# Kernel optimization log

Hardware: AMD Instinct MI355X
Metric: run time of the kernel (lower is better)

## Reference

```python
import jax, jax.numpy as jnp
import numpy as np
from jax import lax

ROI_H, ROI_W = 3, 3          # args.roi_size
MAP_SCALE = 8.0              # args.map_scale
UPS = 8                      # args.upsample_ratio
RADIUS = 8
C_OUT = 5                    # boxes per image
WH = ROI_H * 2 ** 2 + 1      # 13: correlation weight spatial size


def conv2d(x, w, b=None, pad=0):
    y = lax.conv_general_dilated(x, w, (1, 1), [(pad, pad), (pad, pad)],
                                 dimension_numbers=('NCHW', 'OIHW', 'NCHW'))
    return y if b is None else y + b[None, :, None, None]


def resize_ac(x, oh, ow):
    """Bilinear resize with align_corners=True. x: (N,C,H,W) -> (N,C,oh,ow)."""
    H, W = x.shape[2], x.shape[3]
    def grid(n_in, n_out):
        if n_out == 1:
            c = jnp.zeros((1,), x.dtype)
        else:
            c = jnp.arange(n_out, dtype=x.dtype) * ((n_in - 1) / (n_out - 1))
        i0 = jnp.clip(jnp.floor(c).astype(jnp.int32), 0, n_in - 1)
        i1 = jnp.clip(i0 + 1, 0, n_in - 1)
        return i0, i1, c - i0.astype(x.dtype)
    h0, h1, fh = grid(H, oh)
    w0, w1, fw = grid(W, ow)
    xr = x[:, :, h0, :] * (1 - fh)[None, None, :, None] + x[:, :, h1, :] * fh[None, None, :, None]
    return xr[:, :, :, w0] * (1 - fw)[None, None, None, :] + xr[:, :, :, w1] * fw[None, None, None, :]


def roi_pooling(feat, boxes_np, out_size):
    """feat: (N,C,H,W); boxes_np: host int array (N,M,4) [x_min,y_min,width,height].
    Returns (N,M,C,out_h,out_w). Boxes are integer constants, so the
    per-box Python loop traces to fixed shapes (N*M small)."""
    N, M = feat.shape[0], boxes_np.shape[1]
    out = []
    for i in range(N):
        regs = []
        for j in range(M):
            x_min, y_min, width, height = (int(v) for v in boxes_np[i, j])
            region = feat[i:i + 1, :, y_min:y_min + height + 1, x_min:x_min + width + 1]
            scale = max(height, width) / max(out_size)
            nh = max(int(height / scale), 1)
            nw = max(int(width / scale), 1)
            region = resize_ac(region, nh, nw)
            tp = (out_size[0] - nh) // 2
            lp = (out_size[1] - nw) // 2
            pr = jnp.pad(region, ((0, 0), (0, 0), (tp, out_size[0] - nh - tp),
                                  (lp, out_size[1] - nw - lp)))[0]
            regs.append(pr / (1e-6 + pr.sum()))
        out.append(jnp.stack(regs))
    return jnp.stack(out)


def _fpn_fuse(feats, p):
    f = [feats[0]] + [conv2d(x, p['c1x1_w%d' % k], p['c1x1_b%d' % k])
                      for k, x in enumerate(feats[1:])]
    # up_and_add pairs (uses original f list, not cascaded)
    P = [resize_ac(f[i], f[i - 1].shape[2], f[i - 1].shape[3]) + f[i - 1] for i in (3, 2, 1)]
    # NB: original ModuleList([conv]*3) shares ONE smooth conv across all levels
    P = [conv2d(x, p['smooth_w'], p['smooth_b'], pad=1) for x in P]
    P = list(reversed(P)) + [f[3]]
    H, W = P[0].shape[2], P[0].shape[3]
    P = [P[0]] + [resize_ac(x, H, W) for x in P[1:]]
    x = conv2d(jnp.concatenate(P, axis=1), p['fuse_w'], pad=1)
    # BatchNorm with fresh running stats (mean=0, var=1), eps=1e-5
    x = x / jnp.sqrt(jnp.asarray(1.0 + 1e-5, x.dtype)) * p['bn_g'][None, :, None, None] + p['bn_b'][None, :, None, None]
    return jax.nn.relu(x)


def _forward(x0, x1, x2, x3, c1x1_w0, c1x1_b0, c1x1_w1, c1x1_b1, c1x1_w2, c1x1_b2,
             smooth_w, smooth_b, fuse_w, bn_g, bn_b,
             ll_w1, ll_b1, ll_w2, ll_b2, ll_w3, ll_b3,
             of_w1, of_b1, of_w2, of_b2, of_w3, of_b3, x_example):
    p = dict(c1x1_w0=c1x1_w0, c1x1_b0=c1x1_b0, c1x1_w1=c1x1_w1, c1x1_b1=c1x1_b1,
             c1x1_w2=c1x1_w2, c1x1_b2=c1x1_b2, smooth_w=smooth_w, smooth_b=smooth_b,
             fuse_w=fuse_w, bn_g=bn_g, bn_b=bn_b)
    z1 = _fpn_fuse([x0, x1, x2, x3], p)
    B, C_IN, H, W = z1.shape
    # boxes are integer indices -> host constants (matches boxes.long())
    boxes_np = (np.asarray(jax.device_get(x_example)) / MAP_SCALE).astype(np.int64)

    weights, z_e = [], None
    for i in range(3):
        rs = (ROI_H * 2 ** i + 1, ROI_W * 2 ** i + 1)
        z_e = roi_pooling(z1, boxes_np, rs)                     # (B,5,C_IN,rh,rw)
        aug = jnp.concatenate([z_e, z_e[..., ::-1], z_e[..., ::-1, :],
                               z_e[..., ::-1, ::-1]], axis=1)   # (B,20,C_IN,rh,rw)
        ph = (WH - rs[0]) // 2
        pw = (WH - rs[1]) // 2
        weights.append(jnp.pad(aug, ((0, 0), (0, 0), (0, 0),
                                     (ph, WH - rs[0] - ph), (pw, WH - rs[1] - pw))))
    # weights built under torch.no_grad -> constants
    w_all = lax.stop_gradient(jnp.concatenate(weights, axis=1))  # (B,60,C_IN,13,13)

    conv_map = jnp.zeros((B, C_OUT * 12, H, W), z1.dtype)
    corr = jax.vmap(lambda z, w: conv2d(z[None], w, pad=WH // 2)[0])
    for i in range(3):
        res = corr(z1, w_all[:, i * C_OUT * 4:(i + 1) * C_OUT * 4])  # (B,20,H,W)
        # replicate original (buggy) slice conv_map[b, i:i+20] = ...
        conv_map = conv_map.at[:, i:i + C_OUT * 4].set(res)
    atten = conv_map.mean(axis=1, keepdims=True)

    h = jnp.concatenate([conv_map, z1 * atten], axis=1)          # (B,316,H,W)
    h = jax.nn.relu(conv2d(h, ll_w1, ll_b1, pad=1))
    h = jax.nn.relu(conv2d(h, ll_w2, ll_b2, pad=1))
    out1 = jax.nn.relu(conv2d(h, ll_w3, ll_b3))

    o = jax.nn.relu(conv2d(z1, of_w1, of_b1, pad=1))
    o = jax.nn.relu(conv2d(o, of_w2, of_b2, pad=1))
    o = jax.nn.sigmoid(conv2d(o, of_w3, of_b3))
    offset = (MAP_SCALE * o - MAP_SCALE / 2) * RADIUS

    offset = resize_ac(offset, H * UPS, W * UPS)
    out1 = resize_ac(out1, H * UPS, W * UPS)
    return out1, offset, atten, lax.stop_gradient(z_e)


def setup_inputs() -> dict:
    key = jax.random.key(0)
    ks = jax.random.split(key, 20)
    f32 = jnp.float32
    def w(k, shape):
        return jax.random.normal(k, shape, f32) * 0.01  # torch init std=0.01
    inp = {
        'x0': jax.random.normal(ks[0], (2, 256, 64, 64), f32),
        'x1': jax.random.normal(ks[1], (2, 512, 32, 32), f32),
        'x2': jax.random.normal(ks[2], (2, 1024, 16, 16), f32),
        'x3': jax.random.normal(ks[3], (2, 2048, 8, 8), f32),
    }
    # boxes in pixel coords [x_min, y_min, width, height]; image assumed 512px
    xy = jax.random.randint(ks[4], (2, 5, 2), 0, 280)
    wh = jax.random.randint(ks[5], (2, 5, 2), 16, 144)
    inp['x_example'] = jnp.concatenate([xy, wh], axis=-1).astype(f32)
    inp.update(
        c1x1_w0=w(ks[6], (256, 512, 1, 1)), c1x1_b0=jnp.zeros((256,), f32),
        c1x1_w1=w(ks[7], (256, 1024, 1, 1)), c1x1_b1=jnp.zeros((256,), f32),
        c1x1_w2=w(ks[8], (256, 2048, 1, 1)), c1x1_b2=jnp.zeros((256,), f32),
        smooth_w=w(ks[9], (256, 256, 3, 3)), smooth_b=jnp.zeros((256,), f32),
        fuse_w=w(ks[10], (256, 1024, 3, 3)),
        bn_g=jnp.ones((256,), f32), bn_b=jnp.zeros((256,), f32),
        ll_w1=w(ks[11], (64, 316, 3, 3)), ll_b1=jnp.zeros((64,), f32),
        ll_w2=w(ks[12], (64, 64, 3, 3)), ll_b2=jnp.zeros((64,), f32),
        ll_w3=w(ks[13], (1, 64, 1, 1)), ll_b3=jnp.zeros((1,), f32),
        of_w1=w(ks[14], (64, 256, 3, 3)), of_b1=jnp.zeros((64,), f32),
        of_w2=w(ks[15], (64, 64, 3, 3)), of_b2=jnp.zeros((64,), f32),
        of_w3=w(ks[16], (2, 64, 1, 1)), of_b3=jnp.zeros((2,), f32),
    )
    return inp


def reference(x0, x1, x2, x3, x_example, c1x1_w0, c1x1_b0, c1x1_w1, c1x1_b1,
              c1x1_w2, c1x1_b2, smooth_w, smooth_b, fuse_w, bn_g, bn_b,
              ll_w1, ll_b1, ll_w2, ll_b2, ll_w3, ll_b3,
              of_w1, of_b1, of_w2, of_b2, of_w3, of_b3):
    return _forward(x0, x1, x2, x3, c1x1_w0, c1x1_b0, c1x1_w1, c1x1_b1, c1x1_w2,
                    c1x1_b2, smooth_w, smooth_b, fuse_w, bn_g, bn_b,
                    ll_w1, ll_b1, ll_w2, ll_b2, ll_w3, ll_b3,
                    of_w1, of_b1, of_w2, of_b2, of_w3, of_b3, x_example)
```

## Files before the change

kernel.cpp:

```cpp
#include <hip/hip_runtime.h>
#include <math.h>

#define TPB 256
#define TILE 16
#define OCB 8
#define CORR_CS 32

enum { M_BIAS=0, M_BIAS_RELU=1, M_BN_RELU=2, M_SIGAFF=3 };

template<int K>
__global__ __launch_bounds__(TPB)
void conv_k(const float* __restrict__ in, long inb,
            float* __restrict__ out, long outb,
            const float* __restrict__ w,
            const float* __restrict__ a1, const float* __restrict__ a2,
            int Cin, int Cout, int H, int W, int mode, int CS)
{
    constexpr int PAD = K/2;
    constexpr int S = TILE + K - 1;
    __shared__ float tile[S*S];
    __shared__ float wl[OCB*K*K];
    int tilesX = (W + TILE-1)/TILE;
    int tY = blockIdx.x / tilesX, tX = blockIdx.x % tilesX;
    int oc0 = blockIdx.y * OCB;
    int zz = blockIdx.z;
    int cs = zz % CS, b = zz / CS;
    int c0 = (cs*Cin)/CS, c1 = ((cs+1)*Cin)/CS;
    int tid = threadIdx.x;
    int ty = tid / TILE, tx = tid % TILE;
    int y = tY*TILE+ty, x = tX*TILE+tx;
    int oy0 = tY*TILE - PAD, ox0 = tX*TILE - PAD;
    int ocmax = Cout - oc0; if (ocmax > OCB) ocmax = OCB;
    float acc[OCB];
#pragma unroll
    for (int o=0;o<OCB;o++) acc[o]=0.f;
    const float* inp = in + (long)b*inb;
    const int HW = H*W;

    for (int c=c0;c<c1;c++){
        __syncthreads();
        const float* ic = inp + (long)c*HW;
        for (int idx=tid; idx<S*S; idx+=TPB){
            int sy = oy0 + idx/S, sx = ox0 + idx%S;
            tile[idx] = (sy>=0 && sy<H && sx>=0 && sx<W) ? ic[sy*W+sx] : 0.f;
        }
        if (tid < ocmax*(K*K)){
            int o = tid/(K*K), k = tid - o*(K*K);
            wl[o*(K*K)+k] = w[((long)(oc0+o)*Cin + c)*(K*K) + k];
        }
        __syncthreads();
        for (int k=0;k<K*K;k++){
            float xv = tile[(ty + k/K)*S + tx + k%K];
            for (int o=0;o<ocmax;o++)
                acc[o] = fmaf(xv, wl[o*(K*K)+k], acc[o]);
        }
    }

    if (y<H && x<W){
        if (CS==1){
            for (int o=0;o<ocmax;o++){
                int oc = oc0+o;
                float v = acc[o];
                if (mode==M_BIAS) { v += a1[oc]; }
                else if (mode==M_BIAS_RELU) { v += a1[oc]; v = fmaxf(v,0.f); }
                else if (mode==M_BN_RELU) { v = v / sqrtf(1.0f+1e-5f) * a1[oc] + a2[oc]; v = fmaxf(v,0.f); }
                else { v += a1[oc]; float s = 1.f/(1.f+expf(-v)); v = (8.f*s - 4.f)*8.f; }
                out[(long)b*outb + (long)oc*HW + (long)y*W + x] = v;
            }
        } else {
            for (int o=0;o<ocmax;o++)
                out[(((long)(b*CS+cs)*Cout + (oc0+o))*(long)HW) + (long)y*W + x] = acc[o];
        }
    }
}

#define C3S 76
__global__ __launch_bounds__(TPB)
void conv3_64(const float* __restrict__ in, long inb,
              float* __restrict__ out, long outb,
              const float* __restrict__ w,
              const float* __restrict__ a1, const float* __restrict__ a2,
              int Cin, int Cout, int mode, int CS, int wCin, int wskip)
{
    __shared__ __align__(16) float slds[34*C3S];
    __shared__ __align__(16) float wlds[9*4];
    int ytile = blockIdx.x;
    int oc0 = blockIdx.y*4;
    int zz = blockIdx.z;
    int cs = zz % CS, b = zz / CS;
    int c0 = (cs*Cin)/CS, c1 = ((cs+1)*Cin)/CS;
    int tid = threadIdx.x;
    int tx = tid >> 5, ty = tid & 31;
    int y0 = ytile*32;
    const long wstr = (long)wCin*9;

    for (int i=tid;i<34*12;i+=TPB){
        int row=i/12, j=i-row*12;
        int col = (j<4)? j : 64+j;
        slds[row*C3S+col] = 0.f;
    }

    float acc[8][4];
#pragma unroll
    for (int p=0;p<8;p++)
#pragma unroll
        for (int o=0;o<4;o++) acc[p][o]=0.f;

    for (int c=c0;c<c1;++c){
        __syncthreads();
        const float* ic = in + (long)b*inb + ((long)c<<12);
        for (int i=tid;i<544;i+=TPB){
            int row=i>>4, q=i&15;
            int gy = y0-1+row;
            float4 v = make_float4(0.f,0.f,0.f,0.f);
            if (gy>=0 && gy<64) v = *(const float4*)(ic + (gy<<6) + q*4);
            *(float4*)(slds + row*C3S + 4 + q*4) = v;
        }
        int cw = (wskip && c>=22) ? c+38 : c;
        if (tid<36){
            int o=tid/9, k=tid-o*9;
            wlds[k*4+o] = w[(long)(oc0+o)*wstr + (long)cw*9 + k];
        }
        __syncthreads();

#pragma unroll
        for (int r=0;r<3;r++){
            const float* srow = slds + (ty+r)*C3S + tx*8;
            float4 r0 = *(const float4*)(srow);
            float4 r1 = *(const float4*)(srow+4);
            float4 r2 = *(const float4*)(srow+8);
            float4 r3 = *(const float4*)(srow+12);
            float t[10];
            t[0]=r0.w;
            t[1]=r1.x; t[2]=r1.y; t[3]=r1.z; t[4]=r1.w;
            t[5]=r2.x; t[6]=r2.y; t[7]=r2.z; t[8]=r2.w;
            t[9]=r3.x;
#pragma unroll
            for (int k=0;k<3;k++){
                float4 w4 = *(const float4*)(wlds + (r*3+k)*4);
#pragma unroll
                for (int p=0;p<8;p++){
                    acc[p][0] = fmaf(t[p+k], w4.x, acc[p][0]);
                    acc[p][1] = fmaf(t[p+k], w4.y, acc[p][1]);
                    acc[p][2] = fmaf(t[p+k], w4.z, acc[p][2]);
                    acc[p][3] = fmaf(t[p+k], w4.w, acc[p][3]);
                }
            }
        }
    }

    int y = y0+ty, x = tx*8;
    if (CS==1){
#pragma unroll
        for (int o=0;o<4;o++){
            int oc = oc0+o;
            float bb=0.f, gg=1.f;
            if (mode==M_BN_RELU){ gg=a1[oc]; bb=a2[oc]; }
            else { bb=a1[oc]; }
            float v[8];
#pragma unroll
            for (int p=0;p<8;p++){
                float u = acc[p][o];
                if (mode==M_BIAS) u += bb;
                else if (mode==M_BIAS_RELU){ u += bb; u = fmaxf(u,0.f); }
                else if (mode==M_BN_RELU){ u = u / sqrtf(1.0f+1e-5f) * gg + bb; u = fmaxf(u,0.f); }
                v[p] = u;
            }
            float* op = out + (long)b*outb + ((long)oc<<12) + (y<<6) + x;
            *(float4*)(op)   = make_float4(v[0],v[1],v[2],v[3]);
            *(float4*)(op+4) = make_float4(v[4],v[5],v[6],v[7]);
        }
    } else {
#pragma unroll
        for (int o=0;o<4;o++){
            float* op = out + (((long)(b*CS+cs)*Cout + (oc0+o))<<12) + (y<<6) + x;
            *(float4*)(op)   = make_float4(acc[0][o],acc[1][o],acc[2][o],acc[3][o]);
            *(float4*)(op+4) = make_float4(acc[4][o],acc[5][o],acc[6][o],acc[7][o]);
        }
    }
}

__global__ __launch_bounds__(TPB)
void convred_k(const float* __restrict__ part, float* __restrict__ out, long outb,
               const float* __restrict__ a1, const float* __restrict__ a2,
               int Cout, int HW, int CS, int mode)
{
    long total = (long)2*Cout*HW;
    long i = (long)blockIdx.x*TPB + threadIdx.x;
    if (i>=total) return;
    int px = (int)(i % HW); long t = i / HW;
    int oc = (int)(t % Cout); int b = (int)(t / Cout);
    float s = 0.f;
    for (int cs=0;cs<CS;cs++) s += part[(((long)(b*CS+cs)*Cout + oc)*(long)HW) + px];
    if (mode==M_BIAS) s += a1[oc];
    else if (mode==M_BIAS_RELU){ s += a1[oc]; s = fmaxf(s,0.f); }
    else { s = s / sqrtf(1.0f+1e-5f) * a1[oc] + a2[oc]; s = fmaxf(s,0.f); }
    out[(long)b*outb + (long)oc*HW + px] = s;
}

__global__ __launch_bounds__(TPB)
void resize_k(const float* __restrict__ in, long inb, int hi, int wi,
              float* __restrict__ out, long outb, int ho, int wo,
              const float* __restrict__ add, long addb,
              int C, int B, float rh, float rw)
{
    long total = (long)B*C*ho*wo;
    long i = (long)blockIdx.x*TPB + threadIdx.x;
    if (i >= total) return;
    int x = (int)(i % wo); long t = i / wo;
    int y = (int)(t % ho); t /= ho;
    int c = (int)(t % C);  int b = (int)(t / C);
    float cy = (float)y*rh, cx = (float)x*rw;
    int y0 = (int)floorf(cy); if (y0 > hi-1) y0 = hi-1; if (y0 < 0) y0 = 0;
    int x0 = (int)floorf(cx); if (x0 > wi-1) x0 = wi-1; if (x0 < 0) x0 = 0;
    int y1 = y0+1; if (y1 > hi-1) y1 = hi-1;
    int x1 = x0+1; if (x1 > wi-1) x1 = wi-1;
    float fy = cy - (float)y0, fx = cx - (float)x0;
    const float* ib = in + (long)b*inb + (long)c*hi*wi;
    float a = ib[y0*wi+x0], b2 = ib[y0*wi+x1];
    float cc = ib[y1*wi+x0], d = ib[y1*wi+x1];
    float v = (a*(1.f-fy)+cc*fy)*(1.f-fx) + (b2*(1.f-fy)+d*fy)*fx;
    long oidx = (long)b*outb + (long)c*ho*wo + (long)y*wo + x;
    if (add) v += add[(long)b*addb + (long)c*ho*wo + (long)y*wo + x];
    out[oidx] = v;
}

__global__ __launch_bounds__(TPB)
void roi_k(const float* __restrict__ z1, const float* __restrict__ xex,
           float* __restrict__ ze, float* __restrict__ sums,
           int ohw, int M, int C, int H, int W)
{
    int bj = blockIdx.x;
    int b = bj / M;
    int c = threadIdx.x;
    const float* bx = xex + (long)bj*4;
    int x_min = (int)(bx[0]/8.0f);
    int y_min = (int)(bx[1]/8.0f);
    int wdt   = (int)(bx[2]/8.0f);
    int hgt   = (int)(bx[3]/8.0f);
    int mx = hgt > wdt ? hgt : wdt;
    double scale = (double)mx / (double)ohw;
    int nh = (int)((double)hgt / scale); if (nh < 1) nh = 1;
    int nw = (int)((double)wdt / scale); if (nw < 1) nw = 1;
    if (nh > ohw) nh = ohw; if (nw > ohw) nw = ohw;
    int tp = (ohw - nh)/2, lp = (ohw - nw)/2;
    float rh = nh>1 ? (float)((double)hgt/(double)(nh-1)) : 0.f;
    float rw = nw>1 ? (float)((double)wdt/(double)(nw-1)) : 0.f;

    float* zeb = ze + ((long)bj*C + c)*ohw*ohw;
    for (int k=0;k<ohw*ohw;k++) zeb[k] = 0.f;

    const float* src = z1 + ((long)b*C + c)*H*W;
    float ssum = 0.f;
    for (int oy=0;oy<nh;oy++){
        float cy = (float)oy * rh;
        int y0 = (int)floorf(cy); if (y0 > hgt) y0 = hgt; if (y0 < 0) y0 = 0;
        int y1 = y0+1; if (y1 > hgt) y1 = hgt;
        float fy = cy - (float)y0;
        int gy0 = y_min + y0; if (gy0 > H-1) gy0 = H-1;
        int gy1 = y_min + y1; if (gy1 > H-1) gy1 = H-1;
        for (int ox=0;ox<nw;ox++){
            float cx = (float)ox * rw;
            int x0 = (int)floorf(cx); if (x0 > wdt) x0 = wdt; if (x0 < 0) x0 = 0;
            int x1 = x0+1; if (x1 > wdt) x1 = wdt;
            float fx = cx - (float)x0;
            int gx0 = x_min + x0; if (gx0 > W-1) gx0 = W-1;
            int gx1 = x_min + x1; if (gx1 > W-1) gx1 = W-1;
            float a = src[gy0*W+gx0], b2 = src[gy0*W+gx1];
            float cc = src[gy1*W+gx0], d = src[gy1*W+gx1];
            float v = (a*(1.f-fy)+cc*fy)*(1.f-fx) + (b2*(1.f-fy)+d*fy)*fx;
            zeb[(tp+oy)*ohw + lp+ox] = v;
            ssum += v;
        }
    }
    __shared__ float red[TPB];
    red[c] = ssum; __syncthreads();
    for (int s=TPB/2; s>0; s>>=1){
        if (c < s) red[c] += red[c+s];
        __syncthreads();
    }
    if (c==0) sums[bj] = red[0];
}

__global__ __launch_bounds__(TPB)
void norm_k(float* __restrict__ ze, const float* __restrict__ sums,
            int per_bj, long total, float* __restrict__ out2)
{
    long i = (long)blockIdx.x*TPB + threadIdx.x;
    if (i >= total) return;
    int bj = (int)(i / per_bj);
    float v = ze[i] / (1e-6f + sums[bj]);
    ze[i] = v;
    if (out2) out2[i] = v;
}

#define CRS 52
__global__ __launch_bounds__(TPB)
void corr3_k(const float* __restrict__ z1, const float* __restrict__ ze0,
             const float* __restrict__ ze1, const float* __restrict__ ze2,
             float* __restrict__ part)
{
    __shared__ __align__(16) float slds[44*CRS];
    __shared__ __align__(16) float wl[13*16];
    __shared__ float w1l[49];
    __shared__ float w0l[16];
    int tileI = blockIdx.x, job = blockIdx.y;
    int zz = blockIdx.z;
    int b = zz >> 5, cs = zz & 31;
    int x0 = (tileI&1)*32, y0 = (tileI>>1)*32;
    int tid = threadIdx.x, tx = tid&7, ty = tid>>3;
    int c0 = cs*(256/CORR_CS), c1 = c0 + (256/CORR_CS);

    float a[4][4];
#pragma unroll
    for (int f=0;f<4;f++)
#pragma unroll
        for (int p=0;p<4;p++) a[f][p]=0.f;

    for (int c=c0;c<c1;++c){
        __syncthreads();
        const float* ic = z1 + (((long)b*256 + c)<<12);
        for (int i=tid;i<44*44;i+=TPB){
            int row=i/44, col=i-row*44;
            int gy=y0-6+row, gx=x0-6+col;
            slds[row*CRS+col] = (gy>=0&&gy<64&&gx>=0&&gx<64)? ic[(gy<<6)+gx] : 0.f;
        }
        if (job<5){
            if (tid<169){
                wl[(tid/13)*16 + (tid%13)] = ze2[((long)(b*5+job)*256 + c)*169 + tid];
            }
        } else {
            if (tid<49) w1l[tid] = ze1[((long)(b*5)*256 + c)*49 + tid];
            else if (tid<65) w0l[tid-49] = ze0[((long)(b*5)*256 + c)*16 + (tid-49)];
        }
        __syncthreads();

        if (job<5){
            for (int r=0;r<13;r++){
                const float* srow = slds + (ty+r)*CRS + tx*4;
                float4 t0 = *(const float4*)(srow);
                float4 t1 = *(const float4*)(srow+4);
                float4 t2v = *(const float4*)(srow+8);
                float4 t3 = *(const float4*)(srow+12);
                float t[16];
                t[0]=t0.x; t[1]=t0.y; t[2]=t0.z; t[3]=t0.w;
                t[4]=t1.x; t[5]=t1.y; t[6]=t1.z; t[7]=t1.w;
                t[8]=t2v.x; t[9]=t2v.y; t[10]=t2v.z; t[11]=t2v.w;
                t[12]=t3.x; t[13]=t3.y; t[14]=t3.z; t[15]=t3.w;
                const float* wp0 = wl + r*16;
                const float* wp1 = wl + (12-r)*16;
                float4 A0=*(const float4*)(wp0), B0=*(const float4*)(wp0+4),
                       C0=*(const float4*)(wp0+8), D0=*(const float4*)(wp0+12);
                float4 A1=*(const float4*)(wp1), B1=*(const float4*)(wp1+4),
                       C1=*(const float4*)(wp1+8), D1=*(const float4*)(wp1+12);
                float w0r[13] = {A0.x,A0.y,A0.z,A0.w,B0.x,B0.y,B0.z,B0.w,C0.x,C0.y,C0.z,C0.w,D0.x};
                float w1r[13] = {A1.x,A1.y,A1.z,A1.w,B1.x,B1.y,B1.z,B1.w,C1.x,C1.y,C1.z,C1.w,D1.x};
#pragma unroll
                for (int k=0;k<13;k++){
                    float wa = w0r[k], wb = w0r[12-k];
                    float wc = w1r[k], wd = w1r[12-k];
#pragma unroll
                    for (int p=0;p<4;p++){
                        float xv = t[p+k];
                        a[0][p] = fmaf(xv, wa, a[0][p]);
                        a[1][p] = fmaf(xv, wb, a[1][p]);
                        a[2][p] = fmaf(xv, wc, a[2][p]);
                        a[3][p] = fmaf(xv, wd, a[3][p]);
                    }
                }
            }
        } else {
#pragma unroll
            for (int i4=0;i4<4;i4++){
                const float* sr = slds + (ty+4+i4)*CRS + tx*4 + 4;
                float t7[7];
#pragma unroll
                for (int q=0;q<7;q++) t7[q]=sr[q];
#pragma unroll
                for (int t=0;t<4;t++){
                    float wv = w0l[i4*4+t];
#pragma unroll
                    for (int p=0;p<4;p++) a[0][p] = fmaf(t7[p+t], wv, a[0][p]);
                }
            }
#pragma unroll
            for (int i7=0;i7<7;i7++){
                const float* sr = slds + (ty+3+i7)*CRS + tx*4 + 3;
                float t10[10];
#pragma unroll
                for (int q=0;q<10;q++) t10[q]=sr[q];
#pragma unroll
                for (int t=0;t<7;t++){
                    float wv = w1l[i7*7+t];
#pragma unroll
                    for (int p=0;p<4;p++) a[1][p] = fmaf(t10[p+t], wv, a[1][p]);
                }
            }
        }
    }

    int y = y0+ty, x = x0+tx*4;
    long base = (long)(b*CORR_CS+cs)*22;
    if (job<5){
#pragma unroll
        for (int f=0;f<4;f++){
            int oc = 2 + f*5 + job;
            *(float4*)(part + ((base+oc)<<12) + (y<<6) + x) =
                make_float4(a[f][0],a[f][1],a[f][2],a[f][3]);
        }
    } else {
        *(float4*)(part + ((base+0)<<12) + (y<<6) + x) = make_float4(a[0][0],a[0][1],a[0][2],a[0][3]);
        *(float4*)(part + ((base+1)<<12) + (y<<6) + x) = make_float4(a[1][0],a[1][1],a[1][2],a[1][3]);
    }
}

__global__ __launch_bounds__(TPB)
void corrred_k(const float* __restrict__ part, float* __restrict__ cm)
{
    long total = (long)2*22*4096;
    long i = (long)blockIdx.x*TPB + threadIdx.x;
    if (i>=total) return;
    int px = (int)(i & 4095); long t = i >> 12;
    int oc = (int)(t % 22); int b = (int)(t / 22);
    float s = 0.f;
    for (int cs=0;cs<CORR_CS;cs++)
        s += part[(((long)(b*CORR_CS+cs)*22 + oc)<<12) + px];
    cm[((long)(b*22+oc)<<12) + px] = s;
}

__global__ __launch_bounds__(TPB)
void atten_k(const float* __restrict__ cmap, float* __restrict__ att, int B, int HW)
{
    int i = blockIdx.x*TPB + threadIdx.x;
    if (i >= B*HW) return;
    int b = i/HW, p = i%HW;
    float s = 0.f;
    for (int m=0;m<22;m++) s += cmap[((long)(b*22+m))*HW + p];
    att[i] = s * (1.f/60.f);
}

__global__ __launch_bounds__(TPB)
void buildh_k(const float* __restrict__ cmap, const float* __restrict__ z1,
              const float* __restrict__ att, float* __restrict__ h, int B, int HW)
{
    long total = (long)B*278*HW;
    long i = (long)blockIdx.x*TPB + threadIdx.x;
    if (i >= total) return;
    int p = (int)(i % HW); long t = i / HW;
    int ch = (int)(t % 278); int b = (int)(t / 278);
    float v;
    if (ch < 22) v = cmap[((long)(b*22+ch))*HW + p];
    else         v = z1[((long)b*256 + (ch-22))*HW + p] * att[b*HW + p];
    h[i] = v;
}

static inline float acr(int nin, int nout){
    return (float)(((double)(nin-1))/(double)(nout-1));
}

extern "C" void kernel_launch(void* const* d_in, const int* in_sizes, int n_in,
                              void* d_out_v, int out_size, void* d_ws, size_t ws_size,
                              hipStream_t stream)
{
    const float* x0  = (const float*)d_in[0];
    const float* x1  = (const float*)d_in[1];
    const float* x2  = (const float*)d_in[2];
    const float* x3  = (const float*)d_in[3];
    const float* xex = (const float*)d_in[4];
    const float* c1w0=(const float*)d_in[5];  const float* c1b0=(const float*)d_in[6];
    const float* c1w1=(const float*)d_in[7];  const float* c1b1=(const float*)d_in[8];
    const float* c1w2=(const float*)d_in[9];  const float* c1b2=(const float*)d_in[10];
    const float* smw =(const float*)d_in[11]; const float* smb =(const float*)d_in[12];
    const float* fw  =(const float*)d_in[13];
    const float* bng =(const float*)d_in[14]; const float* bnb =(const float*)d_in[15];
    const float* lw1 =(const float*)d_in[16]; const float* lb1 =(const float*)d_in[17];
    const float* lw2 =(const float*)d_in[18]; const float* lb2 =(const float*)d_in[19];
    const float* lw3 =(const float*)d_in[20]; const float* lb3 =(const float*)d_in[21];
    const float* ow1 =(const float*)d_in[22]; const float* ob1 =(const float*)d_in[23];
    const float* ow2 =(const float*)d_in[24]; const float* ob2 =(const float*)d_in[25];
    const float* ow3 =(const float*)d_in[26]; const float* ob3 =(const float*)d_in[27];
    float* dout = (float*)d_out_v;
    float* ws   = (float*)d_ws;

    const int B=2, HW=4096;

    float* f1  = ws;
    float* f2  = f1  + 524288;
    float* f3  = f2  + 131072;
    float* P1  = f3  + 32768;
    float* P2  = P1  + 2097152;
    float* P3  = P2  + 524288;
    float* S2  = P3  + 131072;
    float* S3  = S2  + 524288;
    float* CC  = S3  + 131072;
    float* Z1  = CC  + 8388608;
    float* ZE0 = Z1  + 2097152;
    float* ZE1 = ZE0 + 40960;
    float* ZE2 = ZE1 + 125440;
    float* SUM = ZE2 + 432640;
    float* CM  = SUM + 32;
    float* Hb  = CM  + 180224;
    float* HB1 = Hb  + 2588672;
    float* HB2 = HB1 + 524288;
    float* O164= HB2 + 524288;
    float* OB1 = O164+ 8192;
    float* OB2 = OB1 + 524288;
    float* OFF = OB2 + 524288;
    float* PBF = Hb;
    float* PBC = CC;

    float* out1_dst = dout;
    float* off_dst  = dout + 524288;
    float* att_dst  = dout + 1572864;
    float* ze_dst   = dout + 1581056;

    conv_k<1><<<dim3(4,32,B*2), TPB, 0, stream>>>(x1, 512*1024, PBF, 0, c1w0, nullptr, nullptr, 512,256,32,32, M_BIAS, 2);
    convred_k<<<(524288+TPB-1)/TPB, TPB, 0, stream>>>(PBF, f1, 256*1024, c1b0, nullptr, 256, 1024, 2, M_BIAS);
    conv_k<1><<<dim3(1,32,B*8), TPB, 0, stream>>>(x2, 1024*256, PBF, 0, c1w1, nullptr, nullptr, 1024,256,16,16, M_BIAS, 8);
    convred_k<<<(131072+TPB-1)/TPB, TPB, 0, stream>>>(PBF, f2, 256*256, c1b1, nullptr, 256, 256, 8, M_BIAS);
    conv_k<1><<<dim3(1,32,B*8), TPB, 0, stream>>>(x3, 2048*64, PBF, 0, c1w2, nullptr, nullptr, 2048,256,8,8, M_BIAS, 8);
    convred_k<<<(32768+TPB-1)/TPB, TPB, 0, stream>>>(PBF, f3, 256*64, c1b2, nullptr, 256, 64, 8, M_BIAS);

    resize_k<<<(131072+TPB-1)/TPB, TPB, 0, stream>>>(f3, 256*64, 8,8,   P3, 256*256, 16,16, f2, 256*256, 256, B, acr(8,16), acr(8,16));
    resize_k<<<(524288+TPB-1)/TPB, TPB, 0, stream>>>(f2, 256*256, 16,16, P2, 256*1024, 32,32, f1, 256*1024, 256, B, acr(16,32), acr(16,32));
    resize_k<<<(2097152+TPB-1)/TPB, TPB, 0, stream>>>(f1, 256*1024, 32,32, P1, 256*4096, 64,64, x0, 256*4096, 256, B, acr(32,64), acr(32,64));

    conv3_64<<<dim3(2,64,B*2), TPB, 0, stream>>>(P1, 256*4096, PBF, 0, smw, nullptr, nullptr, 256,256, M_BIAS, 2, 256, 0);
    convred_k<<<(2097152+TPB-1)/TPB, TPB, 0, stream>>>(PBF, CC, 1024*4096, smb, nullptr, 256, 4096, 2, M_BIAS);
    conv_k<3><<<dim3(4,32,B*2), TPB, 0, stream>>>(P2, 256*1024, PBF, 0, smw, nullptr, nullptr, 256,256,32,32, M_BIAS, 2);
    convred_k<<<(524288+TPB-1)/TPB, TPB, 0, stream>>>(PBF, S2, 256*1024, smb, nullptr, 256, 1024, 2, M_BIAS);
    conv_k<3><<<dim3(1,32,B*4), TPB, 0, stream>>>(P3, 256*256, PBF, 0, smw, nullptr, nullptr, 256,256,16,16, M_BIAS, 4);
    convred_k<<<(131072+TPB-1)/TPB, TPB, 0, stream>>>(PBF, S3, 256*256, smb, nullptr, 256, 256, 4, M_BIAS);

    resize_k<<<(2097152+TPB-1)/TPB, TPB, 0, stream>>>(S2, 256*1024, 32,32, CC+256*4096, 1024*4096, 64,64, nullptr,0, 256, B, acr(32,64), acr(32,64));
    resize_k<<<(2097152+TPB-1)/TPB, TPB, 0, stream>>>(S3, 256*256,  16,16, CC+512*4096, 1024*4096, 64,64, nullptr,0, 256, B, acr(16,64), acr(16,64));
    resize_k<<<(2097152+TPB-1)/TPB, TPB, 0, stream>>>(f3, 256*64,   8,8,   CC+768*4096, 1024*4096, 64,64, nullptr,0, 256, B, acr(8,64),  acr(8,64));

    conv3_64<<<dim3(2,64,B*2), TPB, 0, stream>>>(CC, 1024*4096, PBF, 0, fw, nullptr, nullptr, 1024,256, M_BN_RELU, 2, 1024, 0);
    convred_k<<<(2097152+TPB-1)/TPB, TPB, 0, stream>>>(PBF, Z1, 256*4096, bng, bnb, 256, 4096, 2, M_BN_RELU);

    roi_k<<<B*5, TPB, 0, stream>>>(Z1, xex, ZE0, SUM+0,  4,  5, 256, 64, 64);
    roi_k<<<B*5, TPB, 0, stream>>>(Z1, xex, ZE1, SUM+10, 7,  5, 256, 64, 64);
    roi_k<<<B*5, TPB, 0, stream>>>(Z1, xex, ZE2, SUM+20, 13, 5, 256, 64, 64);
    norm_k<<<(40960+TPB-1)/TPB,  TPB, 0, stream>>>(ZE0, SUM+0,  256*16,  40960,  nullptr);
    norm_k<<<(125440+TPB-1)/TPB, TPB, 0, stream>>>(ZE1, SUM+10, 256*49,  125440, nullptr);
    norm_k<<<(432640+TPB-1)/TPB, TPB, 0, stream>>>(ZE2, SUM+20, 256*169, 432640, ze_dst);

    corr3_k<<<dim3(4,6,B*CORR_CS), TPB, 0, stream>>>(Z1, ZE0, ZE1, ZE2, PBC);
    corrred_k<<<(180224+TPB-1)/TPB, TPB, 0, stream>>>(PBC, CM);

    atten_k<<<(B*HW+TPB-1)/TPB, TPB, 0, stream>>>(CM, att_dst, B, HW);

    buildh_k<<<((long)B*278*HW+TPB-1)/TPB, TPB, 0, stream>>>(CM, Z1, att_dst, Hb, B, HW);

    conv3_64<<<dim3(2,16,B*8), TPB, 0, stream>>>(Hb, 278*4096, PBC, 0, lw1, nullptr, nullptr, 278,64, M_BIAS_RELU, 8, 316, 1);
    convred_k<<<(524288+TPB-1)/TPB, TPB, 0, stream>>>(PBC, HB1, 64*4096, lb1, nullptr, 64, 4096, 8, M_BIAS_RELU);
    conv3_64<<<dim3(2,16,B*8), TPB, 0, stream>>>(HB1, 64*4096, PBC, 0, lw2, nullptr, nullptr, 64,64, M_BIAS_RELU, 8, 64, 0);
    convred_k<<<(524288+TPB-1)/TPB, TPB, 0, stream>>>(PBC, HB2, 64*4096, lb2, nullptr, 64, 4096, 8, M_BIAS_RELU);
    conv_k<1><<<dim3(16,1,B), TPB, 0, stream>>>(HB2, 64*4096, O164, 1*4096, lw3, lb3, nullptr, 64,1,64,64, M_BIAS_RELU, 1);

    conv3_64<<<dim3(2,16,B*8), TPB, 0, stream>>>(Z1, 256*4096, PBC, 0, ow1, nullptr, nullptr, 256,64, M_BIAS_RELU, 8, 256, 0);
    convred_k<<<(524288+TPB-1)/TPB, TPB, 0, stream>>>(PBC, OB1, 64*4096, ob1, nullptr, 64, 4096, 8, M_BIAS_RELU);
    conv3_64<<<dim3(2,16,B*8), TPB, 0, stream>>>(OB1, 64*4096, PBC, 0, ow2, nullptr, nullptr, 64,64, M_BIAS_RELU, 8, 64, 0);
    convred_k<<<(524288+TPB-1)/TPB, TPB, 0, stream>>>(PBC, OB2, 64*4096, ob2, nullptr, 64, 4096, 8, M_BIAS_RELU);
    conv_k<1><<<dim3(16,1,B), TPB, 0, stream>>>(OB2, 64*4096, OFF, 2*4096, ow3, ob3, nullptr, 64,2,64,64, M_SIGAFF, 1);

    resize_k<<<(524288+TPB-1)/TPB,  TPB, 0, stream>>>(O164, 4096, 64,64, out1_dst, 262144, 512,512, nullptr,0, 1, B, acr(64,512), acr(64,512));
    resize_k<<<(1048576+TPB-1)/TPB, TPB, 0, stream>>>(OFF,  8192, 64,64, off_dst,  524288, 512,512, nullptr,0, 2, B, acr(64,512), acr(64,512));
}
```

Measured before the change: 3.088 ms.

## Add 128-thread 3x3 conv kernel with 8x8 register tile for 64x64 maps

Adds a new conv3w8 kernel in which each of 128 threads computes 8 output pixels by 8 output channels over a 16-row tile, staging one input channel plus halo and the 8-channel weights in LDS per step. It replaces conv3_64 for the big 64x64 convolutions: smooth, fuse, the first location-layer conv and the first offset conv. The goal is more FMAs per LDS load and a different grid shape (4 row tiles by OC/8). The trade-offs are a large 64-float accumulator per thread and two syncthreads per input channel, which may limit latency hiding.

```diff
diff --git a/kernel.cpp b/kernel.cpp
--- a/kernel.cpp
+++ b/kernel.cpp
@@ -177,6 +177,93 @@
             *(float4*)(op)   = make_float4(acc[0][o],acc[1][o],acc[2][o],acc[3][o]);
             *(float4*)(op+4) = make_float4(acc[4][o],acc[5][o],acc[6][o],acc[7][o]);
         }
+    }
+}
+
+__global__ __launch_bounds__(128)
+void conv3w8(const float* __restrict__ in, long inb,
+             float* __restrict__ out,
+             const float* __restrict__ w,
+             int Cin, int Cout, int CS, int wCin, int wskip)
+{
+    __shared__ __align__(16) float slds[18*C3S];
+    __shared__ __align__(16) float wlds[9*8];
+    int ytile = blockIdx.x;
+    int oc0 = blockIdx.y*8;
+    int zz = blockIdx.z;
+    int cs = zz % CS, b = zz / CS;
+    int c0 = (cs*Cin)/CS, c1 = ((cs+1)*Cin)/CS;
+    int tid = threadIdx.x;
+    int tx = tid & 7, ty = tid >> 3;
+    int y0 = ytile*16;
+    const long wstr = (long)wCin*9;
+
+    for (int i=tid;i<18*12;i+=128){
+        int row=i/12, j=i-row*12;
+        int col = (j<5)? j : 64+j;
+        slds[row*C3S+col] = 0.f;
+    }
+
+    float acc[8][8];
+#pragma unroll
+    for (int p=0;p<8;p++)
+#pragma unroll
+        for (int o=0;o<8;o++) acc[p][o]=0.f;
+
+    for (int c=c0;c<c1;++c){
+        __syncthreads();
+        const float* ic = in + (long)b*inb + ((long)c<<12);
+        for (int i=tid;i<288;i+=128){
+            int row=i>>4, q=i&15;
+            int gy = y0-1+row;
+            float4 v = make_float4(0.f,0.f,0.f,0.f);
+            if (gy>=0 && gy<64) v = *(const float4*)(ic + (gy<<6) + q*4);
+            float* d = slds + row*C3S + 5 + q*4;
+            d[0]=v.x; d[1]=v.y; d[2]=v.z; d[3]=v.w;
+        }
+        int cw = (wskip && c>=22) ? c+38 : c;
+        if (tid<72){
+            int o=tid/9, k=tid-o*9;
+            wlds[k*8+o] = w[(long)(oc0+o)*wstr + (long)cw*9 + k];
+        }
+        __syncthreads();
+
+#pragma unroll
+        for (int r=0;r<3;r++){
+            const float* srow = slds + (ty+r)*C3S + tx*8 + 4;
+            float4 ra = *(const float4*)(srow);
+            float4 rb = *(const float4*)(srow+4);
+            float4 rc = *(const float4*)(srow+8);
+            float t[12];
+            t[0]=ra.x; t[1]=ra.y; t[2]=ra.z; t[3]=ra.w;
+            t[4]=rb.x; t[5]=rb.y; t[6]=rb.z; t[7]=rb.w;
+            t[8]=rc.x; t[9]=rc.y; t[10]=rc.z; t[11]=rc.w;
+#pragma unroll
+            for (int k=0;k<3;k++){
+                float4 wa = *(const float4*)(wlds + (r*3+k)*8);
+                float4 wb = *(const float4*)(wlds + (r*3+k)*8 + 4);
+#pragma unroll
+                for (int p=0;p<8;p++){
+                    float xv = t[p+k];
+                    acc[p][0] = fmaf(xv, wa.x, acc[p][0]);
+                    acc[p][1] = fmaf(xv, wa.y, acc[p][1]);
+                    acc[p][2] = fmaf(xv, wa.z, acc[p][2]);
+                    acc[p][3] = fmaf(xv, wa.w, acc[p][3]);
+                    acc[p][4] = fmaf(xv, wb.x, acc[p][4]);
+                    acc[p][5] = fmaf(xv, wb.y, acc[p][5]);
+                    acc[p][6] = fmaf(xv, wb.z, acc[p][6]);
+                    acc[p][7] = fmaf(xv, wb.w, acc[p][7]);
+                }
+            }
+        }
+    }
+
+    int y = y0+ty, x = tx*8;
+#pragma unroll
+    for (int o=0;o<8;o++){
+        float* op = out + (((long)(b*CS+cs)*Cout + (oc0+o))<<12) + (y<<6) + x;
+        *(float4*)(op)   = make_float4(acc[0][o],acc[1][o],acc[2][o],acc[3][o]);
+        *(float4*)(op+4) = make_float4(acc[4][o],acc[5][o],acc[6][o],acc[7][o]);
     }
 }
 
@@ -525,7 +612,7 @@
     resize_k<<<(524288+TPB-1)/TPB, TPB, 0, stream>>>(f2, 256*256, 16,16, P2, 256*1024, 32,32, f1, 256*1024, 256, B, acr(16,32), acr(16,32));
     resize_k<<<(2097152+TPB-1)/TPB, TPB, 0, stream>>>(f1, 256*1024, 32,32, P1, 256*4096, 64,64, x0, 256*4096, 256, B, acr(32,64), acr(32,64));
 
-    conv3_64<<<dim3(2,64,B*2), TPB, 0, stream>>>(P1, 256*4096, PBF, 0, smw, nullptr, nullptr, 256,256, M_BIAS, 2, 256, 0);
+    conv3w8<<<dim3(4,32,B*2), 128, 0, stream>>>(P1, 256*4096, PBF, smw, 256, 256, 2, 256, 0);
     convred_k<<<(2097152+TPB-1)/TPB, TPB, 0, stream>>>(PBF, CC, 1024*4096, smb, nullptr, 256, 4096, 2, M_BIAS);
     conv_k<3><<<dim3(4,32,B*2), TPB, 0, stream>>>(P2, 256*1024, PBF, 0, smw, nullptr, nullptr, 256,256,32,32, M_BIAS, 2);
     convred_k<<<(524288+TPB-1)/TPB, TPB, 0, stream>>>(PBF, S2, 256*1024, smb, nullptr, 256, 1024, 2, M_BIAS);
@@ -536,7 +623,7 @@
     resize_k<<<(2097152+TPB-1)/TPB, TPB, 0, stream>>>(S3, 256*256,  16,16, CC+512*4096, 1024*4096, 64,64, nullptr,0, 256, B, acr(16,64), acr(16,64));
     resize_k<<<(2097152+TPB-1)/TPB, TPB, 0, stream>>>(f3, 256*64,   8,8,   CC+768*4096, 1024*4096, 64,64, nullptr,0, 256, B, acr(8,64),  acr(8,64));
 
-    conv3_64<<<dim3(2,64,B*2), TPB, 0, stream>>>(CC, 1024*4096, PBF, 0, fw, nullptr, nullptr, 1024,256, M_BN_RELU, 2, 1024, 0);
+    conv3w8<<<dim3(4,32,B*2), 128, 0, stream>>>(CC, 1024*4096, PBF, fw, 1024, 256, 2, 1024, 0);
     convred_k<<<(2097152+TPB-1)/TPB, TPB, 0, stream>>>(PBF, Z1, 256*4096, bng, bnb, 256, 4096, 2, M_BN_RELU);
 
     roi_k<<<B*5, TPB, 0, stream>>>(Z1, xex, ZE0, SUM+0,  4,  5, 256, 64, 64);
@@ -553,13 +640,13 @@
 
     buildh_k<<<((long)B*278*HW+TPB-1)/TPB, TPB, 0, stream>>>(CM, Z1, att_dst, Hb, B, HW);
 
-    conv3_64<<<dim3(2,16,B*8), TPB, 0, stream>>>(Hb, 278*4096, PBC, 0, lw1, nullptr, nullptr, 278,64, M_BIAS_RELU, 8, 316, 1);
+    conv3w8<<<dim3(4,8,B*8), 128, 0, stream>>>(Hb, 278*4096, PBC, lw1, 278, 64, 8, 316, 1);
     convred_k<<<(524288+TPB-1)/TPB, TPB, 0, stream>>>(PBC, HB1, 64*4096, lb1, nullptr, 64, 4096, 8, M_BIAS_RELU);
     conv3_64<<<dim3(2,16,B*8), TPB, 0, stream>>>(HB1, 64*4096, PBC, 0, lw2, nullptr, nullptr, 64,64, M_BIAS_RELU, 8, 64, 0);
     convred_k<<<(524288+TPB-1)/TPB, TPB, 0, stream>>>(PBC, HB2, 64*4096, lb2, nullptr, 64, 4096, 8, M_BIAS_RELU);
     conv_k<1><<<dim3(16,1,B), TPB, 0, stream>>>(HB2, 64*4096, O164, 1*4096, lw3, lb3, nullptr, 64,1,64,64, M_BIAS_RELU, 1);
 
-    conv3_64<<<dim3(2,16,B*8), TPB, 0, stream>>>(Z1, 256*4096, PBC, 0, ow1, nullptr, nullptr, 256,64, M_BIAS_RELU, 8, 256, 0);
+    conv3w8<<<dim3(4,8,B*8), 128, 0, stream>>>(Z1, 256*4096, PBC, ow1, 256, 64, 8, 256, 0);
     convred_k<<<(524288+TPB-1)/TPB, TPB, 0, stream>>>(PBC, OB1, 64*4096, ob1, nullptr, 64, 4096, 8, M_BIAS_RELU);
     conv3_64<<<dim3(2,16,B*8), TPB, 0, stream>>>(OB1, 64*4096, PBC, 0, ow2, nullptr, nullptr, 64,64, M_BIAS_RELU, 8, 64, 0);
     convred_k<<<(524288+TPB-1)/TPB, TPB, 0, stream>>>(PBC, OB2, 64*4096, ob2, nullptr, 64, 4096, 8, M_BIAS_RELU);
```

Result: no change. 3.102 ms (+0.4%).
